# Performance work log

Measured on AMD Instinct MI355X. Metric: run time of the kernel, lower is better.

The kernel has to match this reference:

```python
import jax, jax.numpy as jnp
import numpy as np

DIM = 512
PART = 6
EXP = 4
EPS = 1e-5

def setup_inputs() -> dict:
    key = jax.random.key(0)
    ks = jax.random.split(key, 6)
    B, N = 1024, 162
    x = jax.random.normal(ks[0], (B, N, DIM), dtype=jnp.float32)
    part_tokens = jax.random.normal(ks[1], (PART, DIM), dtype=jnp.float32) * (2.0 / DIM) ** 0.5
    ln_g = jnp.ones((DIM,), dtype=jnp.float32)
    ln_b = jnp.zeros((DIM,), dtype=jnp.float32)
    W1 = jax.random.normal(ks[2], (DIM, EXP * DIM), dtype=jnp.float32) * (1.0 / DIM) ** 0.5
    b1 = jnp.zeros((EXP * DIM,), dtype=jnp.float32)
    W2 = jax.random.normal(ks[3], (EXP * DIM, DIM), dtype=jnp.float32) * (1.0 / (EXP * DIM)) ** 0.5
    b2 = jnp.zeros((DIM,), dtype=jnp.float32)
    return {"x": x, "part_tokens": part_tokens, "ln_g": ln_g, "ln_b": ln_b,
            "W1": W1, "b1": b1, "W2": W2, "b2": b2}

def reference(x, part_tokens, ln_g, ln_b, W1, b1, W2, b2):
    scaling = DIM ** 0.5
    # attention: [P,d] x [B,N,d] -> [B,P,N]
    attn = jnp.einsum('pd,bnd->bpn', part_tokens, x)
    attn = jax.nn.softmax(attn, axis=-1)
    # [B,P,N] x [B,N,d] -> [B,P,d], then post-scale (as in source)
    y = jnp.einsum('bpn,bnd->bpd', attn, x) / scaling
    # FeedForwardBlock: LayerNorm -> Linear -> GELU -> (dropout=identity) -> Linear
    mu = jnp.mean(y, axis=-1, keepdims=True)
    var = jnp.mean(jnp.square(y - mu), axis=-1, keepdims=True)
    h = (y - mu) * jax.lax.rsqrt(var + EPS) * ln_g + ln_b
    h = jax.nn.gelu(h @ W1 + b1, approximate=False)
    return h @ W2 + b2
```

## Files before the change

kernel.cpp:

```cpp
#include <hip/hip_runtime.h>
#include <hip/hip_bf16.h>

constexpr int   DIMC  = 512;
constexpr int   PARTC = 6;
constexpr int   NTOK  = 162;
constexpr float SCALING = 22.62741699796952f;
constexpr float LNEPS   = 1e-5f;

typedef __attribute__((ext_vector_type(8))) short bf16x8;
typedef __attribute__((ext_vector_type(4))) float f32x4;

__global__ __launch_bounds__(256) void transpose_f32_bf16(
    const float* __restrict__ in, __hip_bfloat16* __restrict__ outp, int R, int C)
{
  __shared__ float tile[32][33];
  const int tx = threadIdx.x, ty = threadIdx.y;
  const int bx = blockIdx.x, by = blockIdx.y;
  const int c = bx * 32 + tx;
#pragma unroll
  for (int i = 0; i < 32; i += 8) {
    int r = by * 32 + ty + i;
    tile[ty + i][tx] = in[(size_t)r * C + c];
  }
  __syncthreads();
#pragma unroll
  for (int i = 0; i < 32; i += 8) {
    outp[(size_t)(bx * 32 + ty + i) * R + by * 32 + tx] =
        __float2bfloat16(tile[tx][ty + i]);
  }
}

__global__ __launch_bounds__(256, 3) void attn_ln_k(
    const float* __restrict__ x,
    const float* __restrict__ pt,
    const float* __restrict__ g,
    const float* __restrict__ bta,
    __hip_bfloat16* __restrict__ outp)
{
  const int b = blockIdx.x;
  const int tid = threadIdx.x;
  const int w = tid >> 6;
  const int lane = tid & 63;
  const float* __restrict__ xb = x + (size_t)b * (NTOK * DIMC);

  __shared__ __align__(16) float ulds[2][PARTC][DIMC];
  __shared__ float s_lw[4][PARTC];
  __shared__ float s_red[4][2 * PARTC];

  float4 pA[PARTC], pB[PARTC];
#pragma unroll
  for (int p = 0; p < PARTC; ++p) {
    pA[p] = *(const float4*)(pt + p * DIMC + 8 * lane);
    pB[p] = *(const float4*)(pt + p * DIMC + 8 * lane + 4);
  }

  float u[PARTC][8];
  float l[PARTC];
#pragma unroll
  for (int p = 0; p < PARTC; ++p) {
    l[p] = 0.f;
#pragma unroll
    for (int j = 0; j < 8; ++j) u[p][j] = 0.f;
  }

  for (int n = w; n < NTOK; n += 4) {
    const float* xr = xb + (size_t)n * DIMC + 8 * lane;
    float4 xa = *(const float4*)xr;
    float4 xc = *(const float4*)(xr + 4);

    float acc[PARTC];
#pragma unroll
    for (int p = 0; p < PARTC; ++p) {
      acc[p] = xa.x * pA[p].x + xa.y * pA[p].y + xa.z * pA[p].z + xa.w * pA[p].w
             + xc.x * pB[p].x + xc.y * pB[p].y + xc.z * pB[p].z + xc.w * pB[p].w;
    }
#pragma unroll
    for (int off = 32; off > 0; off >>= 1) {
#pragma unroll
      for (int p = 0; p < PARTC; ++p) acc[p] += __shfl_xor(acc[p], off);
    }
#pragma unroll
    for (int p = 0; p < PARTC; ++p) {
      const float we = __expf(acc[p]);
      l[p] += we;
      u[p][0] += we * xa.x; u[p][1] += we * xa.y;
      u[p][2] += we * xa.z; u[p][3] += we * xa.w;
      u[p][4] += we * xc.x; u[p][5] += we * xc.y;
      u[p][6] += we * xc.z; u[p][7] += we * xc.w;
    }
  }

  if (w >= 2) {
#pragma unroll
    for (int p = 0; p < PARTC; ++p) {
      *(float4*)&ulds[w - 2][p][8 * lane]     = make_float4(u[p][0], u[p][1], u[p][2], u[p][3]);
      *(float4*)&ulds[w - 2][p][8 * lane + 4] = make_float4(u[p][4], u[p][5], u[p][6], u[p][7]);
    }
    if (lane == 0) {
#pragma unroll
      for (int p = 0; p < PARTC; ++p) s_lw[w][p] = l[p];
    }
  }
  __syncthreads();
  if (w < 2) {
#pragma unroll
    for (int p = 0; p < PARTC; ++p) {
      float4 a = *(const float4*)&ulds[w][p][8 * lane];
      float4 c = *(const float4*)&ulds[w][p][8 * lane + 4];
      a.x += u[p][0]; a.y += u[p][1]; a.z += u[p][2]; a.w += u[p][3];
      c.x += u[p][4]; c.y += u[p][5]; c.z += u[p][6]; c.w += u[p][7];
      *(float4*)&ulds[w][p][8 * lane]     = a;
      *(float4*)&ulds[w][p][8 * lane + 4] = c;
    }
    if (lane == 0) {
#pragma unroll
      for (int p = 0; p < PARTC; ++p) s_lw[w][p] = l[p];
    }
  }
  __syncthreads();

  float lt[PARTC];
#pragma unroll
  for (int p = 0; p < PARTC; ++p)
    lt[p] = s_lw[0][p] + s_lw[1][p] + s_lw[2][p] + s_lw[3][p];

  float y0[PARTC], y1[PARTC], s1[PARTC], s2[PARTC];
#pragma unroll
  for (int p = 0; p < PARTC; ++p) {
    const float uu0 = ulds[0][p][2 * tid]     + ulds[1][p][2 * tid];
    const float uu1 = ulds[0][p][2 * tid + 1] + ulds[1][p][2 * tid + 1];
    const float inv = 1.f / (lt[p] * SCALING);
    y0[p] = uu0 * inv;
    y1[p] = uu1 * inv;
    s1[p] = y0[p] + y1[p];
    s2[p] = y0[p] * y0[p] + y1[p] * y1[p];
  }
#pragma unroll
  for (int off = 32; off > 0; off >>= 1) {
#pragma unroll
    for (int p = 0; p < PARTC; ++p) {
      s1[p] += __shfl_xor(s1[p], off);
      s2[p] += __shfl_xor(s2[p], off);
    }
  }
  if (lane == 0) {
#pragma unroll
    for (int p = 0; p < PARTC; ++p) {
      s_red[w][p] = s1[p];
      s_red[w][PARTC + p] = s2[p];
    }
  }
  __syncthreads();

  const float ga0 = g[2 * tid], ga1 = g[2 * tid + 1];
  const float bb0 = bta[2 * tid], bb1 = bta[2 * tid + 1];
  __hip_bfloat16* orow = outp + (size_t)b * PARTC * DIMC;
#pragma unroll
  for (int p = 0; p < PARTC; ++p) {
    float S = s_red[0][p] + s_red[1][p] + s_red[2][p] + s_red[3][p];
    float Q = s_red[0][PARTC + p] + s_red[1][PARTC + p] + s_red[2][PARTC + p] + s_red[3][PARTC + p];
    float mu = S * (1.f / 512.f);
    float var = Q * (1.f / 512.f) - mu * mu;
    float r = rsqrtf(var + LNEPS);
    __hip_bfloat162 hv;
    hv.x = __float2bfloat16((y0[p] - mu) * r * ga0 + bb0);
    hv.y = __float2bfloat16((y1[p] - mu) * r * ga1 + bb1);
    *(__hip_bfloat162*)(orow + p * DIMC + 2 * tid) = hv;
  }
}

template <int BM, int BN, bool GELU>
__global__ __launch_bounds__(256) void gemm_bt(
    const __hip_bfloat16* __restrict__ A,
    const __hip_bfloat16* __restrict__ Bt,
    const float* __restrict__ bias,
    void* __restrict__ Cv,
    int M, int N, int K)
{
  constexpr int BK = 64;
  constexpr int LDT = BK + 16;
  __shared__ __align__(16) unsigned short Al[BM][LDT];
  __shared__ __align__(16) unsigned short Bl[BN][LDT];

  const int tid = threadIdx.x;
  const int w = tid >> 6, lane = tid & 63;
  const int wr = w >> 1, wc = w & 1;
  const int tm = blockIdx.y * BM, tn = blockIdx.x * BN;
  constexpr int FM = BM / 32, FN = BN / 32;

  f32x4 acc[FM][FN];
#pragma unroll
  for (int m = 0; m < FM; ++m)
#pragma unroll
    for (int n = 0; n < FN; ++n) acc[m][n] = (f32x4){0.f, 0.f, 0.f, 0.f};

  const int srow = tid >> 3;
  const int scol = (tid & 7) * 8;

  for (int k0 = 0; k0 < K; k0 += BK) {
    __syncthreads();
#pragma unroll
    for (int r = 0; r < BM / 32; ++r) {
      int row = r * 32 + srow;
      *(int4*)(&Al[row][scol]) =
          *(const int4*)(A + (size_t)(tm + row) * K + k0 + scol);
    }
#pragma unroll
    for (int r = 0; r < BN / 32; ++r) {
      int row = r * 32 + srow;
      *(int4*)(&Bl[row][scol]) =
          *(const int4*)(Bt + (size_t)(tn + row) * K + k0 + scol);
    }
    __syncthreads();

#pragma unroll
    for (int kk = 0; kk < 2; ++kk) {
      const int ko = kk * 32 + (lane >> 4) * 8;
      bf16x8 af[FM], bfr[FN];
#pragma unroll
      for (int m = 0; m < FM; ++m)
        af[m] = *(const bf16x8*)(&Al[wr * (BM / 2) + m * 16 + (lane & 15)][ko]);
#pragma unroll
      for (int n = 0; n < FN; ++n)
        bfr[n] = *(const bf16x8*)(&Bl[wc * (BN / 2) + n * 16 + (lane & 15)][ko]);
#pragma unroll
      for (int m = 0; m < FM; ++m)
#pragma unroll
        for (int n = 0; n < FN; ++n)
          acc[m][n] = __builtin_amdgcn_mfma_f32_16x16x32_bf16(
              af[m], bfr[n], acc[m][n], 0, 0, 0);
    }
  }

  const int cl = lane & 15, rg = (lane >> 4) * 4;
#pragma unroll
  for (int m = 0; m < FM; ++m) {
#pragma unroll
    for (int n = 0; n < FN; ++n) {
      int col = tn + wc * (BN / 2) + n * 16 + cl;
      float bv = bias[col];
#pragma unroll
      for (int r = 0; r < 4; ++r) {
        int row = tm + wr * (BM / 2) + m * 16 + rg + r;
        float v = acc[m][n][r] + bv;
        if (GELU) {
          v = 0.5f * v * (1.f + erff(v * 0.7071067811865476f));
          ((__hip_bfloat16*)Cv)[(size_t)row * N + col] = __float2bfloat16(v);
        } else {
          ((float*)Cv)[(size_t)row * N + col] = v;
        }
      }
    }
  }
}

extern "C" void kernel_launch(void* const* d_in, const int* in_sizes, int n_in,
                              void* d_out, int out_size, void* d_ws, size_t ws_size,
                              hipStream_t stream)
{
  const float* x   = (const float*)d_in[0];
  const float* pt  = (const float*)d_in[1];
  const float* g   = (const float*)d_in[2];
  const float* bta = (const float*)d_in[3];
  const float* W1  = (const float*)d_in[4];
  const float* b1  = (const float*)d_in[5];
  const float* W2  = (const float*)d_in[6];
  const float* b2  = (const float*)d_in[7];
  float* outp = (float*)d_out;

  char* ws = (char*)d_ws;
  __hip_bfloat16* W1T = (__hip_bfloat16*)(ws);
  __hip_bfloat16* W2T = (__hip_bfloat16*)(ws + 2097152);
  __hip_bfloat16* LNO = (__hip_bfloat16*)(ws + 4194304);
  __hip_bfloat16* H   = (__hip_bfloat16*)(ws + 10485760);

  transpose_f32_bf16<<<dim3(2048 / 32, 512 / 32), dim3(32, 8), 0, stream>>>(W1, W1T, 512, 2048);
  transpose_f32_bf16<<<dim3(512 / 32, 2048 / 32), dim3(32, 8), 0, stream>>>(W2, W2T, 2048, 512);

  attn_ln_k<<<1024, 256, 0, stream>>>(x, pt, g, bta, LNO);

  gemm_bt<128, 128, true><<<dim3(2048 / 128, 6144 / 128), 256, 0, stream>>>(
      LNO, W1T, b1, (void*)H, 6144, 2048, 512);

  gemm_bt<128, 64, false><<<dim3(512 / 64, 6144 / 128), 256, 0, stream>>>(
      H, W2T, b2, (void*)outp, 6144, 512, 2048);
}
```

Measured before the change: 188.8 us.

## Split attention over token halves into two blocks and merge before LayerNorm

```diff
diff --git a/kernel.cpp b/kernel.cpp
--- a/kernel.cpp
+++ b/kernel.cpp
@@ -4,6 +4,7 @@
 constexpr int   DIMC  = 512;
 constexpr int   PARTC = 6;
 constexpr int   NTOK  = 162;
+constexpr int   HALF  = 81;
 constexpr float SCALING = 22.62741699796952f;
 constexpr float LNEPS   = 1e-5f;
 
@@ -30,14 +31,15 @@
   }
 }
 
-__global__ __launch_bounds__(256, 3) void attn_ln_k(
+__global__ __launch_bounds__(256, 3) void attn_part_k(
     const float* __restrict__ x,
     const float* __restrict__ pt,
-    const float* __restrict__ g,
-    const float* __restrict__ bta,
-    __hip_bfloat16* __restrict__ outp)
-{
-  const int b = blockIdx.x;
+    float* __restrict__ UP,
+    float* __restrict__ LP)
+{
+  const int bh = blockIdx.x;
+  const int b = bh >> 1;
+  const int base = (bh & 1) * HALF;
   const int tid = threadIdx.x;
   const int w = tid >> 6;
   const int lane = tid & 63;
@@ -45,7 +47,6 @@
 
   __shared__ __align__(16) float ulds[2][PARTC][DIMC];
   __shared__ float s_lw[4][PARTC];
-  __shared__ float s_red[4][2 * PARTC];
 
   float4 pA[PARTC], pB[PARTC];
 #pragma unroll
@@ -63,7 +64,7 @@
     for (int j = 0; j < 8; ++j) u[p][j] = 0.f;
   }
 
-  for (int n = w; n < NTOK; n += 4) {
+  for (int n = base + w; n < base + HALF; n += 4) {
     const float* xr = xb + (size_t)n * DIMC + 8 * lane;
     float4 xa = *(const float4*)xr;
     float4 xc = *(const float4*)(xr + 4);
@@ -119,19 +120,49 @@
   }
   __syncthreads();
 
+  float* __restrict__ up = UP + (size_t)bh * PARTC * DIMC;
+#pragma unroll
+  for (int p = 0; p < PARTC; ++p) {
+    float2 v;
+    v.x = ulds[0][p][2 * tid]     + ulds[1][p][2 * tid];
+    v.y = ulds[0][p][2 * tid + 1] + ulds[1][p][2 * tid + 1];
+    *(float2*)&up[p * DIMC + 2 * tid] = v;
+  }
+  if (tid < PARTC)
+    LP[(size_t)bh * PARTC + tid] =
+        s_lw[0][tid] + s_lw[1][tid] + s_lw[2][tid] + s_lw[3][tid];
+}
+
+__global__ __launch_bounds__(256, 4) void attn_merge_ln_k(
+    const float* __restrict__ UP,
+    const float* __restrict__ LP,
+    const float* __restrict__ g,
+    const float* __restrict__ bta,
+    __hip_bfloat16* __restrict__ outp)
+{
+  const int b = blockIdx.x;
+  const int tid = threadIdx.x;
+  const int w = tid >> 6;
+  const int lane = tid & 63;
+
+  __shared__ float s_red[4][2 * PARTC];
+
+  const float* __restrict__ up0 = UP + (size_t)(2 * b) * PARTC * DIMC;
+  const float* __restrict__ up1 = up0 + PARTC * DIMC;
+
   float lt[PARTC];
 #pragma unroll
   for (int p = 0; p < PARTC; ++p)
-    lt[p] = s_lw[0][p] + s_lw[1][p] + s_lw[2][p] + s_lw[3][p];
+    lt[p] = LP[(size_t)(2 * b) * PARTC + p] + LP[(size_t)(2 * b + 1) * PARTC + p];
 
   float y0[PARTC], y1[PARTC], s1[PARTC], s2[PARTC];
 #pragma unroll
   for (int p = 0; p < PARTC; ++p) {
-    const float uu0 = ulds[0][p][2 * tid]     + ulds[1][p][2 * tid];
-    const float uu1 = ulds[0][p][2 * tid + 1] + ulds[1][p][2 * tid + 1];
+    float2 a = *(const float2*)&up0[p * DIMC + 2 * tid];
+    float2 c = *(const float2*)&up1[p * DIMC + 2 * tid];
     const float inv = 1.f / (lt[p] * SCALING);
-    y0[p] = uu0 * inv;
-    y1[p] = uu1 * inv;
+    y0[p] = (a.x + c.x) * inv;
+    y1[p] = (a.y + c.y) * inv;
     s1[p] = y0[p] + y1[p];
     s2[p] = y0[p] * y0[p] + y1[p] * y1[p];
   }
@@ -273,11 +304,15 @@
   __hip_bfloat16* W2T = (__hip_bfloat16*)(ws + 2097152);
   __hip_bfloat16* LNO = (__hip_bfloat16*)(ws + 4194304);
   __hip_bfloat16* H   = (__hip_bfloat16*)(ws + 10485760);
+  float*          UP  = (float*)(ws + 35651584);
+  float*          LP  = (float*)(ws + 60817408);
 
   transpose_f32_bf16<<<dim3(2048 / 32, 512 / 32), dim3(32, 8), 0, stream>>>(W1, W1T, 512, 2048);
   transpose_f32_bf16<<<dim3(512 / 32, 2048 / 32), dim3(32, 8), 0, stream>>>(W2, W2T, 2048, 512);
 
-  attn_ln_k<<<1024, 256, 0, stream>>>(x, pt, g, bta, LNO);
+  attn_part_k<<<2048, 256, 0, stream>>>(x, pt, UP, LP);
+
+  attn_merge_ln_k<<<1024, 256, 0, stream>>>(UP, LP, g, bta, LNO);
 
   gemm_bt<128, 128, true><<<dim3(2048 / 128, 6144 / 128), 256, 0, stream>>>(
       LNO, W1T, b1, (void*)H, 6144, 2048, 512);
```

After: 190.7 us. Within noise of the previous version (+1.0%).
